# Optimization experiments

Hardware: AMD Instinct MI355X
Metric: run time of the kernel (lower is better)

The kernel has to match this reference:

```python
import jax, jax.numpy as jnp
import numpy as np

N_DELTA, N_THETA, N_GAMMA = 8, 16, 64
HIDDEN = 64
N_STEPS = 20
DT = 0.01
K_INTRA = 1.0   # within-band Kuramoto coupling
K_CROSS = 0.5   # slow-band -> fast-band drive
TWO_PI = 2.0 * np.pi


def _lin(key, fan_in, fan_out):
    s = 1.0 / np.sqrt(fan_in)
    kw, kb = jax.random.split(key)
    w = jax.random.uniform(kw, (fan_in, fan_out), jnp.float32, -s, s)
    b = jax.random.uniform(kb, (fan_out,), jnp.float32, -s, s)
    return w, b


def setup_inputs() -> dict:
    key = jax.random.key(0)
    ks = jax.random.split(key, 12)
    B, N, D_SCENE, D_QUERY = 65536, 8, 16, 60
    scene = jax.random.normal(ks[0], (B, N, D_SCENE), jnp.float32)
    query = jax.random.normal(ks[1], (B, D_QUERY), jnp.float32)
    # per-sample seeded initial oscillator state (phases uniform, band-typical freqs in Hz)
    delta_phase0 = jax.random.uniform(ks[2], (B, N_DELTA), jnp.float32, 0.0, TWO_PI)
    theta_phase0 = jax.random.uniform(ks[3], (B, N_THETA), jnp.float32, 0.0, TWO_PI)
    gamma_phase0 = jax.random.uniform(ks[4], (B, N_GAMMA), jnp.float32, 0.0, TWO_PI)
    delta_freq = jax.random.uniform(ks[5], (B, N_DELTA), jnp.float32, 1.0, 4.0)
    theta_freq = jax.random.uniform(ks[6], (B, N_THETA), jnp.float32, 4.0, 8.0)
    gamma_freq = jax.random.uniform(ks[7], (B, N_GAMMA), jnp.float32, 30.0, 80.0)
    scene_w, scene_b = _lin(ks[8], D_SCENE, N_GAMMA)
    query_w, query_b = _lin(ks[9], D_QUERY, HIDDEN)
    total_osc = N_DELTA + N_THETA + N_GAMMA
    ro_w1, ro_b1 = _lin(ks[10], total_osc + HIDDEN, HIDDEN)
    ro_w2, ro_b2 = _lin(ks[11], HIDDEN, 2)
    return dict(scene=scene, query=query,
                delta_phase0=delta_phase0, theta_phase0=theta_phase0, gamma_phase0=gamma_phase0,
                delta_freq=delta_freq, theta_freq=theta_freq, gamma_freq=gamma_freq,
                scene_w=scene_w, scene_b=scene_b, query_w=query_w, query_b=query_b,
                ro_w1=ro_w1, ro_b1=ro_b1, ro_w2=ro_w2, ro_b2=ro_b2)


def _meanfield(p, a):
    # mean_j a_j*sin(p_j - p_i) computed in O(n) via sin/cos decomposition
    s = jnp.mean(a * jnp.sin(p), axis=-1, keepdims=True)
    c = jnp.mean(a * jnp.cos(p), axis=-1, keepdims=True)
    return jnp.cos(p) * s - jnp.sin(p) * c


def _cross(p_slow, a_slow, p_fast):
    s = jnp.mean(a_slow * jnp.sin(p_slow), axis=-1, keepdims=True)
    c = jnp.mean(a_slow * jnp.cos(p_slow), axis=-1, keepdims=True)
    return jnp.cos(p_fast) * s - jnp.sin(p_fast) * c


def _integrate(pd, ad, pt, at, pg, ag, fd, ft, fg):
    def step(carry, _):
        pd, ad, pt, at, pg, ag = carry
        dpd = TWO_PI * fd + K_INTRA * _meanfield(pd, ad)
        dpt = TWO_PI * ft + K_INTRA * _meanfield(pt, at) + K_CROSS * _cross(pd, ad, pt)
        dpg = TWO_PI * fg + K_INTRA * _meanfield(pg, ag) + K_CROSS * _cross(pt, at, pg)
        dad = ad * (1.0 - ad * ad)   # Stuart-Landau amplitude relaxation
        dat = at * (1.0 - at * at)
        dag = ag * (1.0 - ag * ag)
        new = (pd + DT * dpd, ad + DT * dad,
               pt + DT * dpt, at + DT * dat,
               pg + DT * dpg, ag + DT * dag)
        return new, None
    (pd, ad, pt, at, pg, ag), _ = jax.lax.scan(step, (pd, ad, pt, at, pg, ag), None, length=N_STEPS)
    return ad, at, ag


def reference(scene, query, delta_phase0, theta_phase0, gamma_phase0,
              delta_freq, theta_freq, gamma_freq,
              scene_w, scene_b, query_w, query_b, ro_w1, ro_b1, ro_w2, ro_b2):
    scene_flat = jnp.mean(scene, axis=1)                       # (B, D_scene)
    gamma_init = jax.nn.sigmoid(scene_flat @ scene_w + scene_b)  # (B, n_gamma)
    gamma_init = jax.lax.stop_gradient(gamma_init)             # .detach() in original
    B = scene.shape[0]
    ad0 = jnp.ones((B, N_DELTA), scene.dtype)
    at0 = jnp.ones((B, N_THETA), scene.dtype)
    ad, at, ag = _integrate(delta_phase0, ad0, theta_phase0, at0,
                            gamma_phase0, gamma_init,
                            delta_freq, theta_freq, gamma_freq)
    osc_feat = jnp.concatenate([ad, at, ag], axis=-1)          # (B, 88)
    q_feat = query @ query_w + query_b                         # (B, hidden)
    combined = jnp.concatenate([osc_feat, q_feat], axis=-1)    # (B, 152)
    h = jax.nn.relu(combined @ ro_w1 + ro_b1)
    logits = h @ ro_w2 + ro_b2
    return jax.nn.log_softmax(logits, axis=-1)
```

## Files before the change

### kernel.cpp

```cpp
#include <hip/hip_runtime.h>


#define WS_W12  0
#define WS_WS   7936
#define WS_BS   8960
#define WS_BEFF 9024
#define WS_W2   9088
#define WS_B2   9216
#define WS_TOT  9218

__global__ __launch_bounds__(256) void dtg_prep(
    const float* __restrict__ sw, const float* __restrict__ sb,
    const float* __restrict__ qw, const float* __restrict__ qb,
    const float* __restrict__ w1, const float* __restrict__ b1,
    const float* __restrict__ w2, const float* __restrict__ b2,
    float* __restrict__ ws)
{
  __shared__ float sm[256];
  const int blk = blockIdx.x, tid = threadIdx.x;
  if (blk < 60) {
    const int c = tid & 63, p = tid >> 6;
    float acc = 0.f;
    for (int j = p * 16; j < p * 16 + 16; ++j)
      acc = fmaf(qw[blk * 64 + j], w1[(88 + j) * 64 + c], acc);
    sm[tid] = acc;
    __syncthreads();
    if (tid < 64)
      ws[WS_W12 + blk * 64 + tid] = sm[tid] + sm[64 + tid] + sm[128 + tid] + sm[192 + tid];
  } else if (blk == 60) {
    const int c = tid & 63, p = tid >> 6;
    float acc = 0.f;
    if (p == 0) {
      acc = b1[c];
      for (int r = 0; r < 24; ++r) acc += w1[r * 64 + c];
    }
    for (int j = p * 16; j < p * 16 + 16; ++j)
      acc = fmaf(qb[j], w1[(88 + j) * 64 + c], acc);
    sm[tid] = acc;
    __syncthreads();
    if (tid < 64)
      ws[WS_BEFF + tid] = sm[tid] + sm[64 + tid] + sm[128 + tid] + sm[192 + tid];
  } else if (blk == 61) {
    for (int i = tid; i < 1218; i += 256) {
      if      (i < 1024) ws[WS_WS + i]          = sw[i];
      else if (i < 1088) ws[WS_BS + (i - 1024)] = sb[i - 1024];
      else if (i < 1216) ws[WS_W2 + (i - 1088)] = w2[i - 1088];
      else               ws[WS_B2 + (i - 1216)] = b2[i - 1216];
    }
  } else {
    const int base = (blk - 62) * 2048;
    for (int j = 0; j < 8; ++j) {
      int i = base + tid + 256 * j;
      ws[WS_W12 + 3840 + i] = w1[1536 + i];
    }
  }
}

#define L_X2   9220
#define L_SF   (9220 + 124*68)
#define L_TOT  (17652 + 16*68)

__global__ __launch_bounds__(256) void dtg_main(
    const float* __restrict__ scene,
    const float* __restrict__ query,
    const float* __restrict__ ws,
    float* __restrict__ outf)
{
  __shared__ float lds[L_TOT];
  const int tid = threadIdx.x;
  const int blk = blockIdx.x;

  {
    const float4* src = (const float4*)ws;
    float4* dst = (float4*)lds;
#pragma unroll
    for (int i = 0; i < 9; ++i) {
      int idx = tid + 256 * i;
      dst[idx] = src[idx];
    }
    if (tid < 2) lds[9216 + tid] = ws[9216 + tid];
  }

  {
    const int s = tid >> 2, q = tid & 3;
    const float4* sp = (const float4*)scene + (size_t)blk * 2048;
    float4 a = make_float4(0.f, 0.f, 0.f, 0.f);
#pragma unroll
    for (int n = 0; n < 8; ++n) {
      float4 v = sp[s * 32 + n * 4 + q];
      a.x += v.x; a.y += v.y; a.z += v.z; a.w += v.w;
    }
    lds[L_SF + (4 * q + 0) * 68 + s] = a.x * 0.125f;
    lds[L_SF + (4 * q + 1) * 68 + s] = a.y * 0.125f;
    lds[L_SF + (4 * q + 2) * 68 + s] = a.z * 0.125f;
    lds[L_SF + (4 * q + 3) * 68 + s] = a.w * 0.125f;

    const float4* qp = (const float4*)query + (size_t)blk * 960;
#pragma unroll
    for (int m = 0; m < 4; ++m) {
      int f4i = q + 4 * m;
      if (f4i < 15) {
        float4 v = qp[s * 15 + f4i];
        int k0 = 4 * f4i;
        lds[L_X2 + (k0 + 0) * 68 + s] = v.x;
        lds[L_X2 + (k0 + 1) * 68 + s] = v.y;
        lds[L_X2 + (k0 + 2) * 68 + s] = v.z;
        lds[L_X2 + (k0 + 3) * 68 + s] = v.w;
      }
    }
  }
  __syncthreads();

  const int sgrp = tid >> 4, cgrp = tid & 15;
  const float* Ws   = lds + WS_WS;
  const float* W12  = lds + WS_W12;

  float ga[4][4];
  {
    float4 bsv = *(const float4*)(lds + WS_BS + 4 * cgrp);
#pragma unroll
    for (int si = 0; si < 4; ++si) {
      ga[si][0] = bsv.x; ga[si][1] = bsv.y; ga[si][2] = bsv.z; ga[si][3] = bsv.w;
    }
#pragma unroll
    for (int k = 0; k < 16; ++k) {
      float4 xv = *(const float4*)(lds + L_SF + k * 68 + 4 * sgrp);
      float4 wv = *(const float4*)(Ws + k * 64 + 4 * cgrp);
      const float x[4] = {xv.x, xv.y, xv.z, xv.w};
      const float w[4] = {wv.x, wv.y, wv.z, wv.w};
#pragma unroll
      for (int si = 0; si < 4; ++si)
#pragma unroll
        for (int ci = 0; ci < 4; ++ci)
          ga[si][ci] = fmaf(x[si], w[ci], ga[si][ci]);
    }
  }

#pragma unroll
  for (int si = 0; si < 4; ++si)
#pragma unroll
    for (int ci = 0; ci < 4; ++ci)
      ga[si][ci] = __builtin_amdgcn_rcpf(1.f + __expf(-ga[si][ci]));
  for (int t = 0; t < 20; ++t) {
#pragma unroll
    for (int si = 0; si < 4; ++si)
#pragma unroll
      for (int ci = 0; ci < 4; ++ci) {
        float a = ga[si][ci];
        ga[si][ci] = fmaf(0.01f, a - a * a * a, a);
      }
  }

#pragma unroll
  for (int ci = 0; ci < 4; ++ci) {
    float4 gw = make_float4(ga[0][ci], ga[1][ci], ga[2][ci], ga[3][ci]);
    *(float4*)(lds + L_X2 + (60 + 4 * cgrp + ci) * 68 + 4 * sgrp) = gw;
  }
  __syncthreads();

  float ha[4][4];
  {
    float4 bev = *(const float4*)(lds + WS_BEFF + 4 * cgrp);
#pragma unroll
    for (int si = 0; si < 4; ++si) {
      ha[si][0] = bev.x; ha[si][1] = bev.y; ha[si][2] = bev.z; ha[si][3] = bev.w;
    }
#pragma unroll 4
    for (int k = 0; k < 124; ++k) {
      float4 xv = *(const float4*)(lds + L_X2 + k * 68 + 4 * sgrp);
      float4 wv = *(const float4*)(W12 + k * 64 + 4 * cgrp);
      const float x[4] = {xv.x, xv.y, xv.z, xv.w};
      const float w[4] = {wv.x, wv.y, wv.z, wv.w};
#pragma unroll
      for (int si = 0; si < 4; ++si)
#pragma unroll
        for (int ci = 0; ci < 4; ++ci)
          ha[si][ci] = fmaf(x[si], w[ci], ha[si][ci]);
    }
  }

  float l0[4], l1[4];
  {
    float2 w2c[4];
#pragma unroll
    for (int ci = 0; ci < 4; ++ci)
      w2c[ci] = *(const float2*)(lds + WS_W2 + (4 * cgrp + ci) * 2);
#pragma unroll
    for (int si = 0; si < 4; ++si) {
      float a0 = 0.f, a1 = 0.f;
#pragma unroll
      for (int ci = 0; ci < 4; ++ci) {
        float r = fmaxf(ha[si][ci], 0.f);
        a0 = fmaf(r, w2c[ci].x, a0);
        a1 = fmaf(r, w2c[ci].y, a1);
      }
      l0[si] = a0; l1[si] = a1;
    }
  }
#pragma unroll
  for (int m = 1; m < 16; m <<= 1) {
#pragma unroll
    for (int si = 0; si < 4; ++si) {
      l0[si] += __shfl_xor(l0[si], m);
      l1[si] += __shfl_xor(l1[si], m);
    }
  }
  if (cgrp == 0) {
    const float bb0 = lds[WS_B2 + 0], bb1 = lds[WS_B2 + 1];
    const int base = blk * 64 + 4 * sgrp;
    float r[8];
#pragma unroll
    for (int si = 0; si < 4; ++si) {
      float a0 = l0[si] + bb0, a1 = l1[si] + bb1;
      float mx  = fmaxf(a0, a1);
      float e0  = __expf(a0 - mx), e1 = __expf(a1 - mx);
      float lse = mx + __logf(e0 + e1);
      r[2 * si] = a0 - lse; r[2 * si + 1] = a1 - lse;
    }
    float4* op = (float4*)(outf + 2 * base);
    op[0] = make_float4(r[0], r[1], r[2], r[3]);
    op[1] = make_float4(r[4], r[5], r[6], r[7]);
  }
}

extern "C" void kernel_launch(void* const* d_in, const int* in_sizes, int n_in,
                              void* d_out, int out_size, void* d_ws, size_t ws_size,
                              hipStream_t stream)
{
  const float* scene = (const float*)d_in[0];
  const float* query = (const float*)d_in[1];
  const float* sw = (const float*)d_in[8];
  const float* sb = (const float*)d_in[9];
  const float* qw = (const float*)d_in[10];
  const float* qb = (const float*)d_in[11];
  const float* w1 = (const float*)d_in[12];
  const float* b1 = (const float*)d_in[13];
  const float* w2 = (const float*)d_in[14];
  const float* b2 = (const float*)d_in[15];
  float* ws = (float*)d_ws;
  const int B = in_sizes[0] / 128;

  hipLaunchKernelGGL(dtg_prep, dim3(64), dim3(256), 0, stream,
                     sw, sb, qw, qb, w1, b1, w2, b2, ws);
  hipLaunchKernelGGL(dtg_main, dim3(B / 64), dim3(256), 0, stream,
                     scene, query, ws, (float*)d_out);
}
```

Before: 149.6 us.

## Read weights directly from global memory instead of staging them in LDS

The per-block copy of roughly 37 KB of weights into shared memory is removed. The GEMM loops now read weight float4s straight from global memory (sw, the folded query weights in the workspace, and w1 rows 24 onward), which should hit in L2/L1 since every block shares them. The prep kernel shrinks to computing only the folded query weights and the effective bias. LDS use drops to about 38 KB and launch bounds request 4 blocks per CU for higher occupancy, at the cost of global-load latency inside the inner FMA loops.

```diff
diff --git a/kernel.cpp b/kernel.cpp
--- a/kernel.cpp
+++ b/kernel.cpp
@@ -1,34 +1,26 @@
 #include <hip/hip_runtime.h>
 
 
-#define WS_W12  0
-#define WS_WS   7936
-#define WS_BS   8960
-#define WS_BEFF 9024
-#define WS_W2   9088
-#define WS_B2   9216
-#define WS_TOT  9218
+#define WS_WQ    0
+#define WS_BEFF  3840
 
 __global__ __launch_bounds__(256) void dtg_prep(
-    const float* __restrict__ sw, const float* __restrict__ sb,
     const float* __restrict__ qw, const float* __restrict__ qb,
     const float* __restrict__ w1, const float* __restrict__ b1,
-    const float* __restrict__ w2, const float* __restrict__ b2,
     float* __restrict__ ws)
 {
   __shared__ float sm[256];
   const int blk = blockIdx.x, tid = threadIdx.x;
+  const int c = tid & 63, p = tid >> 6;
   if (blk < 60) {
-    const int c = tid & 63, p = tid >> 6;
     float acc = 0.f;
     for (int j = p * 16; j < p * 16 + 16; ++j)
       acc = fmaf(qw[blk * 64 + j], w1[(88 + j) * 64 + c], acc);
     sm[tid] = acc;
     __syncthreads();
     if (tid < 64)
-      ws[WS_W12 + blk * 64 + tid] = sm[tid] + sm[64 + tid] + sm[128 + tid] + sm[192 + tid];
-  } else if (blk == 60) {
-    const int c = tid & 63, p = tid >> 6;
+      ws[WS_WQ + blk * 64 + tid] = sm[tid] + sm[64 + tid] + sm[128 + tid] + sm[192 + tid];
+  } else {
     float acc = 0.f;
     if (p == 0) {
       acc = b1[c];
@@ -40,46 +32,34 @@
     __syncthreads();
     if (tid < 64)
       ws[WS_BEFF + tid] = sm[tid] + sm[64 + tid] + sm[128 + tid] + sm[192 + tid];
-  } else if (blk == 61) {
-    for (int i = tid; i < 1218; i += 256) {
-      if      (i < 1024) ws[WS_WS + i]          = sw[i];
-      else if (i < 1088) ws[WS_BS + (i - 1024)] = sb[i - 1024];
-      else if (i < 1216) ws[WS_W2 + (i - 1088)] = w2[i - 1088];
-      else               ws[WS_B2 + (i - 1216)] = b2[i - 1216];
-    }
-  } else {
-    const int base = (blk - 62) * 2048;
-    for (int j = 0; j < 8; ++j) {
-      int i = base + tid + 256 * j;
-      ws[WS_W12 + 3840 + i] = w1[1536 + i];
-    }
   }
 }
 
-#define L_X2   9220
-#define L_SF   (9220 + 124*68)
-#define L_TOT  (17652 + 16*68)
-
-__global__ __launch_bounds__(256) void dtg_main(
+#define L_X2   0
+#define L_SF   (124 * 68)
+#define L_TOT  (L_SF + 16 * 68)
+
+#define KSTEP(ACC, XV, WV)                                                     \
+  { const float x_[4] = {(XV).x, (XV).y, (XV).z, (XV).w};                      \
+    const float w_[4] = {(WV).x, (WV).y, (WV).z, (WV).w};                      \
+    _Pragma("unroll") for (int si_ = 0; si_ < 4; ++si_)                        \
+      _Pragma("unroll") for (int ci_ = 0; ci_ < 4; ++ci_)                      \
+        ACC[si_][ci_] = fmaf(x_[si_], w_[ci_], ACC[si_][ci_]); }
+
+__global__ __launch_bounds__(256, 4) void dtg_main(
     const float* __restrict__ scene,
     const float* __restrict__ query,
+    const float* __restrict__ sw,
+    const float* __restrict__ sb,
+    const float* __restrict__ w1,
+    const float* __restrict__ w2,
+    const float* __restrict__ b2,
     const float* __restrict__ ws,
     float* __restrict__ outf)
 {
   __shared__ float lds[L_TOT];
   const int tid = threadIdx.x;
   const int blk = blockIdx.x;
-
-  {
-    const float4* src = (const float4*)ws;
-    float4* dst = (float4*)lds;
-#pragma unroll
-    for (int i = 0; i < 9; ++i) {
-      int idx = tid + 256 * i;
-      dst[idx] = src[idx];
-    }
-    if (tid < 2) lds[9216 + tid] = ws[9216 + tid];
-  }
 
   {
     const int s = tid >> 2, q = tid & 3;
@@ -112,27 +92,22 @@
   __syncthreads();
 
   const int sgrp = tid >> 4, cgrp = tid & 15;
-  const float* Ws   = lds + WS_WS;
-  const float* W12  = lds + WS_W12;
+  const float4* swp = (const float4*)sw;
+  const float4* wqp = (const float4*)(ws + WS_WQ);
+  const float4* w1p = (const float4*)(w1 + 24 * 64);
 
   float ga[4][4];
   {
-    float4 bsv = *(const float4*)(lds + WS_BS + 4 * cgrp);
+    float4 bsv = ((const float4*)sb)[cgrp];
 #pragma unroll
     for (int si = 0; si < 4; ++si) {
       ga[si][0] = bsv.x; ga[si][1] = bsv.y; ga[si][2] = bsv.z; ga[si][3] = bsv.w;
     }
-#pragma unroll
+#pragma unroll 4
     for (int k = 0; k < 16; ++k) {
       float4 xv = *(const float4*)(lds + L_SF + k * 68 + 4 * sgrp);
-      float4 wv = *(const float4*)(Ws + k * 64 + 4 * cgrp);
-      const float x[4] = {xv.x, xv.y, xv.z, xv.w};
-      const float w[4] = {wv.x, wv.y, wv.z, wv.w};
-#pragma unroll
-      for (int si = 0; si < 4; ++si)
-#pragma unroll
-        for (int ci = 0; ci < 4; ++ci)
-          ga[si][ci] = fmaf(x[si], w[ci], ga[si][ci]);
+      float4 wv = swp[k * 16 + cgrp];
+      KSTEP(ga, xv, wv)
     }
   }
 
@@ -160,22 +135,22 @@
 
   float ha[4][4];
   {
-    float4 bev = *(const float4*)(lds + WS_BEFF + 4 * cgrp);
+    float4 bev = *(const float4*)(ws + WS_BEFF + 4 * cgrp);
 #pragma unroll
     for (int si = 0; si < 4; ++si) {
       ha[si][0] = bev.x; ha[si][1] = bev.y; ha[si][2] = bev.z; ha[si][3] = bev.w;
     }
 #pragma unroll 4
-    for (int k = 0; k < 124; ++k) {
+    for (int k = 0; k < 60; ++k) {
       float4 xv = *(const float4*)(lds + L_X2 + k * 68 + 4 * sgrp);
-      float4 wv = *(const float4*)(W12 + k * 64 + 4 * cgrp);
-      const float x[4] = {xv.x, xv.y, xv.z, xv.w};
-      const float w[4] = {wv.x, wv.y, wv.z, wv.w};
-#pragma unroll
-      for (int si = 0; si < 4; ++si)
-#pragma unroll
-        for (int ci = 0; ci < 4; ++ci)
-          ha[si][ci] = fmaf(x[si], w[ci], ha[si][ci]);
+      float4 wv = wqp[k * 16 + cgrp];
+      KSTEP(ha, xv, wv)
+    }
+#pragma unroll 4
+    for (int k = 0; k < 64; ++k) {
+      float4 xv = *(const float4*)(lds + L_X2 + (60 + k) * 68 + 4 * sgrp);
+      float4 wv = w1p[k * 16 + cgrp];
+      KSTEP(ha, xv, wv)
     }
   }
 
@@ -184,7 +159,7 @@
     float2 w2c[4];
 #pragma unroll
     for (int ci = 0; ci < 4; ++ci)
-      w2c[ci] = *(const float2*)(lds + WS_W2 + (4 * cgrp + ci) * 2);
+      w2c[ci] = ((const float2*)w2)[4 * cgrp + ci];
 #pragma unroll
     for (int si = 0; si < 4; ++si) {
       float a0 = 0.f, a1 = 0.f;
@@ -206,7 +181,7 @@
     }
   }
   if (cgrp == 0) {
-    const float bb0 = lds[WS_B2 + 0], bb1 = lds[WS_B2 + 1];
+    const float bb0 = b2[0], bb1 = b2[1];
     const int base = blk * 64 + 4 * sgrp;
     float r[8];
 #pragma unroll
@@ -240,8 +215,8 @@
   float* ws = (float*)d_ws;
   const int B = in_sizes[0] / 128;
 
-  hipLaunchKernelGGL(dtg_prep, dim3(64), dim3(256), 0, stream,
-                     sw, sb, qw, qb, w1, b1, w2, b2, ws);
+  hipLaunchKernelGGL(dtg_prep, dim3(61), dim3(256), 0, stream,
+                     qw, qb, w1, b1, ws);
   hipLaunchKernelGGL(dtg_main, dim3(B / 64), dim3(256), 0, stream,
-                     scene, query, ws, (float*)d_out);
+                     scene, query, sw, sb, w1, w2, b2, ws, (float*)d_out);
 }
```

New measurement: 153.2 us. 1.02x slower.
